# Kernel tuning notes

Hardware: AMD Instinct MI355X
Metric: run time of the kernel (lower is better)

## Reference

```python
import jax, jax.numpy as jnp
import numpy as np

EPS = 1e-6


def setup_inputs() -> dict:
    key = jax.random.key(0)
    kq, kk, kv = jax.random.split(key, 3)
    B, H, S, D = 4, 16, 4096, 64
    Q = jax.random.normal(kq, (B, H, S, D), dtype=jnp.float32)
    K = jax.random.normal(kk, (B, H, S, D), dtype=jnp.float32)
    V = jax.random.normal(kv, (B, H, S, D), dtype=jnp.float32)
    mask = jnp.ones((B, S), dtype=bool)
    return {"Q": Q, "K": K, "V": V, "mask": mask}


def reference(Q, K, V, mask):
    # Feature map: relu(sinh(x)), applied to Q and K
    Qf = jax.nn.relu(jnp.sinh(Q))            # [B,H,S,D]
    Kf = jax.nn.relu(jnp.sinh(K))            # [B,H,S,D]
    # Zero out padded key positions: mask is [B,S]
    Kf = Kf * mask[:, None, :, None].astype(Kf.dtype)
    # K^T V outer product over sequence: [B,H,D,D]
    attn_inter = jnp.einsum('bhsd,bhse->bhde', Kf, V)
    # Q (K^T V): [B,H,S,D]
    attn_weights = jnp.einsum('bhqd,bhde->bhqe', Qf, attn_inter)
    # Normalizer: Q . sum_s |K_masked| (Kf is nonneg after relu, abs kept for fidelity)
    k_sum = jnp.abs(Kf).sum(axis=2)          # [B,H,D]
    norm = jnp.einsum('bhqd,bhd->bhq', Qf, k_sum)[..., None]  # [B,H,S,1]
    norm = jnp.maximum(norm, EPS)
    return attn_weights / norm
```

## Files before the change

kernel.cpp:

```cpp
#include <hip/hip_runtime.h>
#include <hip/hip_bf16.h>
#include <cstdint>

#define SEQ  4096
#define DIM  64
#define NBH  64
#define FEPS 1e-6f
#define MSTRIDE 4160

typedef __attribute__((ext_vector_type(8))) short bf16x8;
typedef __attribute__((ext_vector_type(4))) float f32x4;

__device__ __forceinline__ float featmap(float x) {
    return x > 0.0f ? 0.5f * (__expf(x) - __expf(-x)) : 0.0f;
}

__device__ __forceinline__ short f2bf(float x) {
    unsigned int u = __float_as_uint(x);
    u += 0x7fffu + ((u >> 16) & 1u);
    return (short)(u >> 16);
}

__global__ __launch_bounds__(256, 4) void k_phase1(
    const float* __restrict__ K, const float* __restrict__ V,
    const int* __restrict__ mask, float* __restrict__ partM,
    int nchunk, int rows_per_chunk)
{
    const int chunk = blockIdx.x;
    const int bh    = blockIdx.y;
    const int b     = bh >> 4;
    const int tid   = threadIdx.x;
    const int wave  = tid >> 6;
    const int lane  = tid & 63;
    const int r     = lane & 15;
    const int g     = lane >> 4;

    const float* Kb = K + (size_t)bh * SEQ * DIM;
    const float* Vb = V + (size_t)bh * SEQ * DIM;
    const int*   mb = mask + (size_t)b * SEQ;

    f32x4 acc[4];
    #pragma unroll
    for (int nt = 0; nt < 4; ++nt) acc[nt] = (f32x4){0.f, 0.f, 0.f, 0.f};
    float ksp = 0.0f;

    const int s0  = chunk * rows_per_chunk;
    const int nks = rows_per_chunk >> 5;

    for (int ks = 0; ks < nks; ++ks) {
        const int srow = s0 + ks * 32 + g * 8;
        const float* ka = Kb + (size_t)srow * DIM + wave * 16 + r;
        const float* va = Vb + (size_t)srow * DIM + r;
        const int*   ma = mb + srow;

        bf16x8 af;
        #pragma unroll
        for (int j = 0; j < 8; ++j) {
            float kf = featmap(ka[(size_t)j * DIM]);
            kf = ma[j] ? kf : 0.0f;
            ksp += kf;
            af[j] = f2bf(kf);
        }

        bf16x8 bf[4];
        #pragma unroll
        for (int j = 0; j < 8; ++j)
            #pragma unroll
            for (int nt = 0; nt < 4; ++nt)
                bf[nt][j] = f2bf(va[(size_t)j * DIM + nt * 16]);

        #pragma unroll
        for (int nt = 0; nt < 4; ++nt)
            acc[nt] = __builtin_amdgcn_mfma_f32_16x16x32_bf16(
                af, bf[nt], acc[nt], 0, 0, 0);
    }

    float* dst = partM + (size_t)(bh * nchunk + chunk) * MSTRIDE;
    #pragma unroll
    for (int nt = 0; nt < 4; ++nt)
        #pragma unroll
        for (int j = 0; j < 4; ++j)
            dst[(wave * 16 + g * 4 + j) * 64 + nt * 16 + r] = acc[nt][j];

    ksp += __shfl_xor(ksp, 16);
    ksp += __shfl_xor(ksp, 32);
    if (lane < 16) dst[4096 + wave * 16 + lane] = ksp;
}

__global__ __launch_bounds__(256) void k_reduce(
    const float* __restrict__ partM, float* __restrict__ finalM, int nchunk)
{
    const int bh  = blockIdx.y;
    const int tid = threadIdx.x;
    const float4* src = (const float4*)(partM + (size_t)bh * nchunk * MSTRIDE);
    float4* dst = (float4*)(finalM + (size_t)bh * MSTRIDE);
    const int qend = blockIdx.x * 260 + 260;
    for (int q = blockIdx.x * 260 + tid; q < qend; q += 256) {
        float4 s = src[q];
        for (int c = 1; c < nchunk; ++c) {
            float4 t = src[(size_t)c * (MSTRIDE / 4) + q];
            s.x += t.x; s.y += t.y; s.z += t.z; s.w += t.w;
        }
        dst[q] = s;
    }
}

__global__ __launch_bounds__(256, 4) void k_phase2(
    const float* __restrict__ Q, const float* __restrict__ finalM,
    float* __restrict__ out)
{
    const int bh   = blockIdx.y;
    const int tid  = threadIdx.x;
    const int wave = tid >> 6;
    const int lane = tid & 63;
    const int r    = lane & 15;
    const int g    = lane >> 4;

    const float* Mb = finalM + (size_t)bh * MSTRIDE;

    bf16x8 bfr[4][2];
    float  ksl[2][8];
    #pragma unroll
    for (int kk = 0; kk < 2; ++kk)
        #pragma unroll
        for (int j = 0; j < 8; ++j) {
            const int d = kk*32 + g*8 + j;
            ksl[kk][j] = Mb[4096 + d];
            #pragma unroll
            for (int nt = 0; nt < 4; ++nt)
                bfr[nt][kk][j] = f2bf(Mb[d*64 + nt*16 + r]);
        }

    const int q0 = blockIdx.x * 64 + wave * 16;
    const float* Qrow = Q + (size_t)bh * SEQ * DIM + (size_t)(q0 + r) * DIM;

    bf16x8 afr[2];
    float z = 0.0f;
    #pragma unroll
    for (int kk = 0; kk < 2; ++kk) {
        float4 x0 = *(const float4*)(Qrow + kk*32 + g*8);
        float4 x1 = *(const float4*)(Qrow + kk*32 + g*8 + 4);
        const float qf[8] = {featmap(x0.x), featmap(x0.y), featmap(x0.z), featmap(x0.w),
                             featmap(x1.x), featmap(x1.y), featmap(x1.z), featmap(x1.w)};
        #pragma unroll
        for (int j = 0; j < 8; ++j) {
            z = fmaf(qf[j], ksl[kk][j], z);
            afr[kk][j] = f2bf(qf[j]);
        }
    }
    z += __shfl_xor(z, 16);
    z += __shfl_xor(z, 32);

    f32x4 acc[4];
    #pragma unroll
    for (int nt = 0; nt < 4; ++nt) acc[nt] = (f32x4){0.f, 0.f, 0.f, 0.f};
    #pragma unroll
    for (int kk = 0; kk < 2; ++kk)
        #pragma unroll
        for (int nt = 0; nt < 4; ++nt)
            acc[nt] = __builtin_amdgcn_mfma_f32_16x16x32_bf16(
                afr[kk], bfr[nt][kk], acc[nt], 0, 0, 0);

    float rinv[4];
    #pragma unroll
    for (int j = 0; j < 4; ++j) {
        const float zc = __shfl(z, g*4 + j);
        rinv[j] = 1.0f / fmaxf(zc, FEPS);
    }
    float* Ob = out + (size_t)bh * SEQ * DIM;
    #pragma unroll
    for (int nt = 0; nt < 4; ++nt)
        #pragma unroll
        for (int j = 0; j < 4; ++j)
            Ob[(size_t)(q0 + g*4 + j) * DIM + nt*16 + r] = acc[nt][j] * rinv[j];
}

extern "C" void kernel_launch(void* const* d_in, const int* in_sizes, int n_in,
                              void* d_out, int out_size, void* d_ws, size_t ws_size,
                              hipStream_t stream) {
    const float* Q    = (const float*)d_in[0];
    const float* K    = (const float*)d_in[1];
    const float* V    = (const float*)d_in[2];
    const int*   mask = (const int*)d_in[3];
    float* out = (float*)d_out;
    float* ws  = (float*)d_ws;

    int nchunk = 16;
    while (nchunk > 1 &&
           ws_size < (size_t)(NBH * nchunk + NBH) * MSTRIDE * sizeof(float))
        nchunk >>= 1;
    const int rows = SEQ / nchunk;

    float* partM  = ws;
    float* finalM = ws + (size_t)NBH * nchunk * MSTRIDE;

    k_phase1<<<dim3(nchunk, NBH), 256, 0, stream>>>(K, V, mask, partM, nchunk, rows);
    k_reduce<<<dim3(4, NBH), 256, 0, stream>>>(partM, finalM, nchunk);
    k_phase2<<<dim3(64, NBH), 256, 0, stream>>>(Q, finalM, out);
}
```

Measured before the change: 247.5 us.

## Stage K/V tiles through double-buffered LDS with vectorized coalesced loads

Phase 1 previously had each lane read strided scalar K and V values straight from global memory, with every wave redundantly converting the full V tile. Threads now load float4 rows, apply the feature map and mask once, pack pairs of rows into bf16 pairs, and write them transposed into a padded, double-buffered LDS tile. The MFMA operands are then read from LDS, and the next tile's global loads are issued before the current tile's compute. The key-sum reduction moves to LDS as well. This adds LDS traffic and a barrier per 32-row tile.

```diff
diff --git a/kernel.cpp b/kernel.cpp
--- a/kernel.cpp
+++ b/kernel.cpp
@@ -7,6 +7,7 @@
 #define NBH  64
 #define FEPS 1e-6f
 #define MSTRIDE 4160
+#define PITCH 20
 
 typedef __attribute__((ext_vector_type(8))) short bf16x8;
 typedef __attribute__((ext_vector_type(4))) float f32x4;
@@ -15,10 +16,13 @@
     return x > 0.0f ? 0.5f * (__expf(x) - __expf(-x)) : 0.0f;
 }
 
-__device__ __forceinline__ short f2bf(float x) {
+__device__ __forceinline__ unsigned int f2bf_u(float x) {
     unsigned int u = __float_as_uint(x);
     u += 0x7fffu + ((u >> 16) & 1u);
-    return (short)(u >> 16);
+    return u >> 16;
+}
+__device__ __forceinline__ unsigned int pack2(float lo, float hi) {
+    return f2bf_u(lo) | (f2bf_u(hi) << 16);
 }
 
 __global__ __launch_bounds__(256, 4) void k_phase1(
@@ -34,45 +38,72 @@
     const int lane  = tid & 63;
     const int r     = lane & 15;
     const int g     = lane >> 4;
+    const int p     = tid & 15;
+    const int d0    = (tid >> 4) * 4;
+
+    __shared__ unsigned int lds[5120];
 
     const float* Kb = K + (size_t)bh * SEQ * DIM;
     const float* Vb = V + (size_t)bh * SEQ * DIM;
     const int*   mb = mask + (size_t)b * SEQ;
 
+    const int s0    = chunk * rows_per_chunk;
+    const int ntile = rows_per_chunk >> 5;
+
     f32x4 acc[4];
     #pragma unroll
     for (int nt = 0; nt < 4; ++nt) acc[nt] = (f32x4){0.f, 0.f, 0.f, 0.f};
-    float ksp = 0.0f;
-
-    const int s0  = chunk * rows_per_chunk;
-    const int nks = rows_per_chunk >> 5;
-
-    for (int ks = 0; ks < nks; ++ks) {
-        const int srow = s0 + ks * 32 + g * 8;
-        const float* ka = Kb + (size_t)srow * DIM + wave * 16 + r;
-        const float* va = Vb + (size_t)srow * DIM + r;
-        const int*   ma = mb + srow;
-
-        bf16x8 af;
-        #pragma unroll
-        for (int j = 0; j < 8; ++j) {
-            float kf = featmap(ka[(size_t)j * DIM]);
-            kf = ma[j] ? kf : 0.0f;
-            ksp += kf;
-            af[j] = f2bf(kf);
-        }
-
-        bf16x8 bf[4];
-        #pragma unroll
-        for (int j = 0; j < 8; ++j)
-            #pragma unroll
-            for (int nt = 0; nt < 4; ++nt)
-                bf[nt][j] = f2bf(va[(size_t)j * DIM + nt * 16]);
-
-        #pragma unroll
-        for (int nt = 0; nt < 4; ++nt)
-            acc[nt] = __builtin_amdgcn_mfma_f32_16x16x32_bf16(
-                af, bf[nt], acc[nt], 0, 0, 0);
+    float ksum4[4] = {0.f, 0.f, 0.f, 0.f};
+
+    float4 k0, k1, v0, v1;
+    int2   mm;
+
+    auto LOAD = [&](int t) {
+        const int s = s0 + t * 32 + 2 * p;
+        k0 = *(const float4*)(Kb + (size_t)s       * DIM + d0);
+        k1 = *(const float4*)(Kb + (size_t)(s + 1) * DIM + d0);
+        v0 = *(const float4*)(Vb + (size_t)s       * DIM + d0);
+        v1 = *(const float4*)(Vb + (size_t)(s + 1) * DIM + d0);
+        mm = *(const int2*)(mb + s);
+    };
+
+    auto STORE = [&](int buf) {
+        unsigned int* KT = lds + buf * 2560;
+        unsigned int* VT = KT + 1280;
+        const float ka[4] = {k0.x, k0.y, k0.z, k0.w};
+        const float kb[4] = {k1.x, k1.y, k1.z, k1.w};
+        const float va[4] = {v0.x, v0.y, v0.z, v0.w};
+        const float vb[4] = {v1.x, v1.y, v1.z, v1.w};
+        #pragma unroll
+        for (int i = 0; i < 4; ++i) {
+            float f0 = mm.x ? featmap(ka[i]) : 0.0f;
+            float f1 = mm.y ? featmap(kb[i]) : 0.0f;
+            ksum4[i] += f0 + f1;
+            KT[(d0 + i) * PITCH + p] = pack2(f0, f1);
+            VT[(d0 + i) * PITCH + p] = pack2(va[i], vb[i]);
+        }
+    };
+
+    auto COMPUTE = [&](int buf) {
+        const unsigned int* KT = lds + buf * 2560;
+        const unsigned int* VT = KT + 1280;
+        const bf16x8 af = *(const bf16x8*)&KT[(wave * 16 + r) * PITCH + 4 * g];
+        #pragma unroll
+        for (int nt = 0; nt < 4; ++nt) {
+            const bf16x8 bf = *(const bf16x8*)&VT[(nt * 16 + r) * PITCH + 4 * g];
+            acc[nt] = __builtin_amdgcn_mfma_f32_16x16x32_bf16(af, bf, acc[nt], 0, 0, 0);
+        }
+    };
+
+    LOAD(0);
+    STORE(0);
+    __syncthreads();
+    for (int t = 0; t < ntile; ++t) {
+        const int cur = t & 1;
+        if (t + 1 < ntile) LOAD(t + 1);
+        COMPUTE(cur);
+        if (t + 1 < ntile) STORE(cur ^ 1);
+        __syncthreads();
     }
 
     float* dst = partM + (size_t)(bh * nchunk + chunk) * MSTRIDE;
@@ -82,9 +113,16 @@
         for (int j = 0; j < 4; ++j)
             dst[(wave * 16 + g * 4 + j) * 64 + nt * 16 + r] = acc[nt][j];
 
-    ksp += __shfl_xor(ksp, 16);
-    ksp += __shfl_xor(ksp, 32);
-    if (lane < 16) dst[4096 + wave * 16 + lane] = ksp;
+    float* kr = (float*)lds;
+    #pragma unroll
+    for (int i = 0; i < 4; ++i) kr[(d0 + i) * 16 + p] = ksum4[i];
+    __syncthreads();
+    if (tid < 64) {
+        float s = 0.0f;
+        #pragma unroll
+        for (int q = 0; q < 16; ++q) s += kr[tid * 16 + q];
+        dst[4096 + tid] = s;
+    }
 }
 
 __global__ __launch_bounds__(256) void k_reduce(
@@ -128,7 +166,7 @@
             ksl[kk][j] = Mb[4096 + d];
             #pragma unroll
             for (int nt = 0; nt < 4; ++nt)
-                bfr[nt][kk][j] = f2bf(Mb[d*64 + nt*16 + r]);
+                bfr[nt][kk][j] = (short)f2bf_u(Mb[d*64 + nt*16 + r]);
         }
 
     const int q0 = blockIdx.x * 64 + wave * 16;
@@ -145,7 +183,7 @@
         #pragma unroll
         for (int j = 0; j < 8; ++j) {
             z = fmaf(qf[j], ksl[kk][j], z);
-            afr[kk][j] = f2bf(qf[j]);
+            afr[kk][j] = (short)f2bf_u(qf[j]);
         }
     }
     z += __shfl_xor(z, 16);
```

New measurement: 249.5 us. Within noise of the previous version (+0.8%).
